# Performance work log

Hardware: AMD Instinct MI355X
Metric: run time of the kernel (lower is better)

## Reference

```python
import jax, jax.numpy as jnp
import numpy as np

NUM_NODES = 100000
NUM_EDGES = 1600000
NUM_GRAPHS = 1000
NUM_REP = 16
R_DIM = 16
N_SCALARS = 16
N_CLASSES = 6
N_LAYERS = 3
L_MAX = 1
EPS = 1e-8


def get_rot(v):
    """2x2 SO(2) rotation from 2D vector angle, L_max=1. v:[n,2] -> [n,1,2,2]."""
    theta = jnp.arctan2(v[:, 1], v[:, 0])
    c, s = jnp.cos(theta), jnp.sin(theta)
    R = jnp.stack([jnp.stack([c, -s], -1), jnp.stack([s, c], -1)], -2)  # [n,2,2]
    return R[:, None]  # [n, L_max=1, 2, 2]


def bessel(d, number=R_DIM, end=1.0):
    """Bessel radial basis sqrt(2/end)*sin(n*pi*d/end)/d. d:[E] -> [E,number]."""
    n = jnp.arange(1, number + 1, dtype=d.dtype)
    d_safe = d[:, None] + EPS
    return jnp.sqrt(2.0 / end) * jnp.sin(n * jnp.pi * d[:, None] / end) / d_safe


def seg_sum(x, idx, n):
    return jax.ops.segment_sum(x, idx, num_segments=n)


def setup_inputs() -> dict:
    key = jax.random.key(0)
    ks = jax.random.split(key, 20)
    pos = jax.random.normal(ks[0], (NUM_NODES, 2), dtype=jnp.float32)
    edge_index = jax.random.randint(ks[1], (2, NUM_EDGES), 0, NUM_NODES)
    batch = jnp.sort(jax.random.randint(ks[2], (NUM_NODES,), 0, NUM_GRAPHS))
    s = 0.1
    return {
        "pos": pos,
        "W_emb_rot": s * jax.random.normal(ks[3], (NUM_REP, L_MAX, 2), jnp.float32),
        "w_s_emb": s * jax.random.normal(ks[4], (N_SCALARS,), jnp.float32),
        "b_s_emb": jnp.zeros((N_SCALARS,), jnp.float32),
        "Wg": s * jax.random.normal(ks[5], (N_LAYERS, R_DIM, NUM_REP), jnp.float32),
        "bg": jnp.zeros((N_LAYERS, NUM_REP), jnp.float32),
        "Wmix": s * jax.random.normal(ks[6], (N_LAYERS, NUM_REP, NUM_REP), jnp.float32),
        "Wgate": s * jax.random.normal(ks[7], (N_LAYERS, N_SCALARS, NUM_REP), jnp.float32),
        "bgate": jnp.zeros((N_LAYERS, NUM_REP), jnp.float32),
        "Ws1": s * jax.random.normal(ks[8], (N_LAYERS, N_SCALARS + R_DIM, N_SCALARS), jnp.float32),
        "bs1": jnp.zeros((N_LAYERS, N_SCALARS), jnp.float32),
        "W1": s * jax.random.normal(ks[9], (N_SCALARS + NUM_REP * L_MAX * 2, 3 * (N_SCALARS + NUM_REP * L_MAX * 2)), jnp.float32),
        "b1": jnp.zeros((3 * (N_SCALARS + NUM_REP * L_MAX * 2),), jnp.float32),
        "W2": s * jax.random.normal(ks[10], (3 * (N_SCALARS + NUM_REP * L_MAX * 2), N_CLASSES), jnp.float32),
        "b2": jnp.zeros((N_CLASSES,), jnp.float32),
        "edge_index": edge_index,
        "batch": batch,
    }


def reference(pos, W_emb_rot, w_s_emb, b_s_emb, Wg, bg, Wmix, Wgate, bgate,
              Ws1, bs1, W1, b1, W2, b2, edge_index, batch):
    N = pos.shape[0]
    # --- geometry under no_grad in torch ---
    posg = jax.lax.stop_gradient(pos)
    cnt = seg_sum(jnp.ones((N,), posg.dtype), batch, NUM_GRAPHS)
    mean = seg_sum(posg, batch, NUM_GRAPHS) / jnp.maximum(cnt, 1.0)[:, None]
    posg = posg - mean[batch]
    rot_theta = get_rot(posg)                        # [N,1,2,2]
    row, col = edge_index[0], edge_index[1]
    edge_vec = posg[row] - posg[col]                 # [E,2]
    rot = get_rot(edge_vec)                          # [E,1,2,2]
    dist = jnp.linalg.norm(edge_vec, axis=1)         # [E]

    dist_emb = bessel(dist)                          # [E,r_dim]

    # --- edge embedding -> node features ---
    e_rot = jnp.einsum('eklm,jkm->ejkl', rot, W_emb_rot)      # [E,rep,1,2]
    deg = jnp.maximum(seg_sum(jnp.ones((row.shape[0],), pos.dtype), row, N), 1.0)
    x_rot = seg_sum(e_rot, row, N) / deg[:, None, None, None]  # [N,rep,1,2]
    d_mean = seg_sum(dist, row, N) / deg
    x_s = jax.nn.leaky_relu(d_mean[:, None] * w_s_emb[None, :] + b_s_emb)  # [N,ns]

    rot_inv = jnp.swapaxes(rot, -1, -2)
    # --- EqBlocks: gather -> rotate-in -> radial mix -> rotate-out -> scatter ---
    for i in range(N_LAYERS):
        local = jnp.einsum('eklm,ejkm->ejkl', rot_inv, x_rot[col])   # [E,rep,1,2]
        g = dist_emb @ Wg[i] + bg[i]                                 # [E,rep]
        local = jnp.einsum('ij,ejkl->eikl', Wmix[i], local) * g[:, :, None, None]
        msg = jnp.einsum('eklm,ejkm->ejkl', rot, local)              # [E,rep,1,2]
        agg = seg_sum(msg, row, N) / deg[:, None, None, None]
        gate = jax.nn.sigmoid(x_s @ Wgate[i] + bgate[i])             # [N,rep]
        x_rot = x_rot + agg * gate[:, :, None, None]
        msg_s = jax.nn.leaky_relu(
            jnp.concatenate([x_s[col], dist_emb], axis=1) @ Ws1[i] + bs1[i])
        x_s = x_s + seg_sum(msg_s, row, N) / deg[:, None]

    # --- SO2OutU (faithful to given source) ---
    rot_theta_inv = jnp.swapaxes(rot_theta, -1, -2)                  # [N,1,2,2]
    x_out = jnp.einsum('njkm,nkml->njkl', x_rot, rot_theta_inv)      # [N,rep,1,2]
    x_cat = jnp.concatenate([x_s, x_out.reshape(N, -1)], axis=1)    # [N,48]
    u = jax.nn.leaky_relu(x_cat @ W1 + b1) @ W2 + b2                 # [N,n_classes]
    return seg_sum(u, batch, NUM_GRAPHS)                             # [G,n_classes]
```

## Files before the change

kernel.cpp:

```cpp
#include <hip/hip_runtime.h>
#include <hip/hip_fp16.h>
#include <math.h>

#define NREP 16
#define RDIM 16
#define NS   16
#define NC   6
#define H1   144
#define DBINS 64
#define TILE 4096
#define P2CAP 10240

static __device__ __forceinline__ float leaky(float v) { return v > 0.0f ? v : 0.01f * v; }

__global__ void k_gsum_count(const float* __restrict__ pos, const int* __restrict__ batch,
                             int N, float* __restrict__ gsum, float* __restrict__ gcnt,
                             const int* __restrict__ ei, int E, int* __restrict__ cnt) {
  int t = threadIdx.x;
  int e = blockIdx.x * 256 + t;
  if (e < E) atomicAdd(&cnt[ei[e]], 1);

  __shared__ float bx[320], by[320], bc[320];
  int start = blockIdx.x * 256;
  if (start >= N) return;
  int n = start + t;
  int b0 = batch[min(start, N - 1)];
  int span = batch[min(start + 255, N - 1)] - b0;
  bool useLds = (span < 320);
  if (useLds) {
    for (int i = t; i <= span; i += 256) { bx[i] = 0.f; by[i] = 0.f; bc[i] = 0.f; }
    __syncthreads();
    if (n < N) {
      int rb = batch[n] - b0;
      atomicAdd(&bx[rb], pos[2 * n + 0]);
      atomicAdd(&by[rb], pos[2 * n + 1]);
      atomicAdd(&bc[rb], 1.0f);
    }
    __syncthreads();
    for (int i = t; i <= span; i += 256) {
      if (bc[i] != 0.0f) {
        atomicAdd(&gsum[2 * (b0 + i) + 0], bx[i]);
        atomicAdd(&gsum[2 * (b0 + i) + 1], by[i]);
        atomicAdd(&gcnt[b0 + i], bc[i]);
      }
    }
  } else if (n < N) {
    int b = batch[n];
    atomicAdd(&gsum[2 * b + 0], pos[2 * n + 0]);
    atomicAdd(&gsum[2 * b + 1], pos[2 * n + 1]);
    atomicAdd(&gcnt[b], 1.0f);
  }
}

__global__ void k_center_dhist_scan1(
    const float* __restrict__ pos, const int* __restrict__ batch, int N,
    const float* __restrict__ gsum, const float* __restrict__ gcnt,
    float* __restrict__ posc, float* __restrict__ cthn, float* __restrict__ sthn,
    const int* __restrict__ cnt, int* __restrict__ dhist,
    int* __restrict__ off, int* __restrict__ bsum) {
  __shared__ int lh[DBINS];
  __shared__ int sd[1024];
  int t = threadIdx.x;
  int i = blockIdx.x * 1024 + t;
  if (t < DBINS) lh[t] = 0;
  int v = (i < N) ? cnt[i] : 0;
  sd[t] = v;
  if (i < N) {
    int b = batch[i];
    float invc = 1.0f / fmaxf(gcnt[b], 1.0f);
    float px = pos[2 * i + 0] - gsum[2 * b + 0] * invc;
    float py = pos[2 * i + 1] - gsum[2 * b + 1] * invc;
    posc[2 * i + 0] = px;
    posc[2 * i + 1] = py;
    float r = sqrtf(px * px + py * py);
    if (r > 0.0f) { cthn[i] = px / r; sthn[i] = py / r; }
    else          { cthn[i] = 1.0f;  sthn[i] = 0.0f; }
  }
  __syncthreads();
  if (i < N) atomicAdd(&lh[min(v, DBINS - 1)], 1);
  for (int o = 1; o < 1024; o <<= 1) {
    int u = (t >= o) ? sd[t - o] : 0;
    __syncthreads();
    sd[t] += u;
    __syncthreads();
  }
  if (i < N) off[i] = sd[t] - v;
  if (t == 1023) bsum[blockIdx.x] = sd[1023];
  if (t < DBINS && lh[t] > 0) atomicAdd(&dhist[t], lh[t]);
}

__global__ void k_dscan_scan2(const int* __restrict__ dhist, int* __restrict__ dcur,
                              int* __restrict__ bsum, int nb) {
  __shared__ int s1[DBINS];
  __shared__ int s2[1024];
  int t = threadIdx.x;
  int v1 = (t < DBINS) ? dhist[t] : 0;
  if (t < DBINS) s1[t] = v1;
  int v2 = (t < nb) ? bsum[t] : 0;
  s2[t] = v2;
  __syncthreads();
  for (int o = 1; o < 1024; o <<= 1) {
    int u1 = (o < DBINS && t >= o && t < DBINS) ? s1[t - o] : 0;
    int u2 = (t >= o) ? s2[t - o] : 0;
    __syncthreads();
    if (o < DBINS && t < DBINS) s1[t] += u1;
    s2[t] += u2;
    __syncthreads();
  }
  if (t < DBINS) dcur[t] = s1[t] - v1;
  if (t < nb) bsum[t] = s2[t] - v2;
}

__global__ void k_dfill_scan3(int* __restrict__ off, const int* __restrict__ bsum,
                              int N, int E,
                              const int* __restrict__ cnt, int* __restrict__ dcur,
                              int* __restrict__ perm, int* __restrict__ cursor,
                              int* __restrict__ bcur) {
  int t = threadIdx.x;
  int i = blockIdx.x * 1024 + t;
  if (i < N) {
    int ov = off[i] + bsum[blockIdx.x];
    off[i] = ov;
    cursor[i] = ov;
    if ((i & 255) == 0) bcur[i >> 8] = ov;
  }
  if (i == N) off[N] = E;

  __shared__ int lh[DBINS];
  __shared__ int base[DBINS];
  if (t < DBINS) lh[t] = 0;
  __syncthreads();
  int b = 0, lr = 0;
  if (i < N) {
    b = min(cnt[i], DBINS - 1);
    lr = atomicAdd(&lh[b], 1);
  }
  __syncthreads();
  if (t < DBINS && lh[t] > 0) base[t] = atomicAdd(&dcur[t], lh[t]);
  __syncthreads();
  if (i < N) perm[base[b] + lr] = i;
}

__global__ void __launch_bounds__(256) k_part1(
    const int* __restrict__ ei, int E,
    int* __restrict__ bcur, long long* __restrict__ ebuf) {
  __shared__ int hist[512], lofs[512], gbase[512], pc[512];
  __shared__ long long stg[TILE];
  __shared__ unsigned short bkt[TILE];
  int t = threadIdx.x;
  int base = blockIdx.x * TILE;
  int cntt = min(TILE, E - base);
  for (int i = t; i < 512; i += 256) { hist[i] = 0; pc[i] = 0; }
  __syncthreads();
  int r[16], c[16];
#pragma unroll
  for (int i = 0; i < 16; i++) {
    int e = base + t + i * 256;
    r[i] = -1;
    if (e < E) {
      r[i] = ei[e];
      c[i] = ei[E + e];
      atomicAdd(&hist[r[i] >> 8], 1);
    }
  }
  __syncthreads();
  lofs[t] = hist[t]; lofs[t + 256] = hist[t + 256];
  __syncthreads();
  for (int o = 1; o < 512; o <<= 1) {
    int a0 = (t >= o) ? lofs[t - o] : 0;
    int a1 = lofs[t + 256 - o];
    __syncthreads();
    lofs[t] += a0; lofs[t + 256] += a1;
    __syncthreads();
  }
  int e0 = lofs[t] - hist[t], e1 = lofs[t + 256] - hist[t + 256];
  __syncthreads();
  lofs[t] = e0; lofs[t + 256] = e1;
  __syncthreads();
  for (int i = t; i < 512; i += 256)
    if (hist[i] > 0) gbase[i] = atomicAdd(&bcur[i], hist[i]);
  __syncthreads();
#pragma unroll
  for (int i = 0; i < 16; i++) {
    if (r[i] >= 0) {
      int b = r[i] >> 8;
      int l = lofs[b] + atomicAdd(&pc[b], 1);
      stg[l] = ((long long)r[i] << 32) | (unsigned int)c[i];
      bkt[l] = (unsigned short)b;
    }
  }
  __syncthreads();
  for (int j = t; j < cntt; j += 256) {
    int b = bkt[j];
    ebuf[gbase[b] + (j - lofs[b])] = stg[j];
  }
}

__global__ void __launch_bounds__(256) k_part2(
    const int* __restrict__ off, int N, const long long* __restrict__ ebuf,
    int* __restrict__ cursor, int* __restrict__ adj) {
  __shared__ int lcur[256];
  __shared__ int ladj[P2CAP];
  int t = threadIdx.x;
  int r0 = blockIdx.x << 8;
  int rend = min(r0 + 256, N);
  int abeg = off[r0];
  int aend = off[rend];
  int sz = aend - abeg;
  lcur[t] = (r0 + t < N) ? (off[r0 + t] - abeg) : 0;
  __syncthreads();
  if (sz <= P2CAP) {
    for (int j = abeg + t; j < aend; j += 256) {
      long long p = ebuf[j];
      int cl = (int)(unsigned int)(p & 0xffffffffLL);
      int rr = (int)(p >> 32);
      int l = atomicAdd(&lcur[rr - r0], 1);
      ladj[l] = cl;
    }
    __syncthreads();
    for (int j = t; j < sz; j += 256) adj[abeg + j] = ladj[j];
  } else {
    for (int j = abeg + t; j < aend; j += 256) {
      long long p = ebuf[j];
      int cl = (int)(unsigned int)(p & 0xffffffffLL);
      int rr = (int)(p >> 32);
      int l = atomicAdd(&cursor[rr], 1);
      adj[l] = cl;
    }
  }
}

__global__ void __launch_bounds__(256) k_init16(
    int N, const int* __restrict__ off, const int* __restrict__ adj,
    const float* __restrict__ posc, float2* __restrict__ spc,
    const float* __restrict__ Wer, const float* __restrict__ wse, const float* __restrict__ bse,
    const float* __restrict__ Wmix, const float* __restrict__ Ws1, const float* __restrict__ bs1,
    const float* __restrict__ Wgate, const float* __restrict__ bgate,
    float* __restrict__ xr, float* __restrict__ xs, uint2* __restrict__ yzg) {
  int idx = blockIdx.x * 256 + threadIdx.x;
  int n = idx >> 4, r = idx & 15;
  if (n >= N) return;
  int a = off[n], b = off[n + 1];
  float px = posc[2 * n + 0], py = posc[2 * n + 1];
  float C = 0.f, S = 0.f, D = 0.f;
  for (int k = a + r; k < b; k += 16) {
    int cl = adj[k];
    float dx = px - posc[2 * cl + 0];
    float dy = py - posc[2 * cl + 1];
    float d = sqrtf(dx * dx + dy * dy);
    float sp, cp;
    sincospif(d, &sp, &cp);
    float spp = 1.41421356237309515f * sp / (d + 1e-8f);
    spc[k] = make_float2(spp, 2.0f * cp);
    if (d > 0.0f) {
      float inv = 1.0f / d;
      C += dx * inv;
      S += dy * inv;
    } else {
      C += 1.0f;
    }
    D += d;
  }
#pragma unroll
  for (int o = 1; o < 16; o <<= 1) {
    C += __shfl_xor(C, o, 16);
    S += __shfl_xor(S, o, 16);
    D += __shfl_xor(D, o, 16);
  }
  float id = 1.0f / fmaxf((float)(b - a), 1.0f);
  C *= id; S *= id;
  float dm = D * id;
  float w0 = Wer[2 * r], w1 = Wer[2 * r + 1];
  float2 x;
  x.x = C * w0 - S * w1;
  x.y = S * w0 + C * w1;
  ((float2*)xr)[(size_t)n * 16 + r] = x;
  float s_new = leaky(dm * wse[r] + bse[r]);
  xs[(size_t)n * 16 + r] = s_new;

  float wmxn[16], wsan[16], wgtn[16];
#pragma unroll
  for (int q = 0; q < 16; q++) wmxn[q] = Wmix[r * 16 + q];
#pragma unroll
  for (int q = 0; q < 16; q++) wsan[q] = Ws1[q * 16 + r];
#pragma unroll
  for (int q = 0; q < 16; q++) wgtn[q] = Wgate[q * 16 + r];
  float y0 = 0.f, y1 = 0.f;
  float z = bs1[r], gtn = bgate[r];
#pragma unroll
  for (int j = 0; j < 16; j++) {
    float xj0 = __shfl(x.x, j, 16);
    float xj1 = __shfl(x.y, j, 16);
    float sj  = __shfl(s_new, j, 16);
    y0 += wmxn[j] * xj0;
    y1 += wmxn[j] * xj1;
    z  += wsan[j] * sj;
    gtn += wgtn[j] * sj;
  }
  gtn = 1.0f / (1.0f + __expf(-gtn));
  __half2 hA = __floats2half2_rn(y0, y1);
  __half2 hB = __floats2half2_rn(z, gtn);
  uint2 w2;
  w2.x = *(unsigned int*)&hA;
  w2.y = *(unsigned int*)&hB;
  yzg[(size_t)n * 16 + r] = w2;
}

__global__ void __launch_bounds__(256) k_layer(
    int N, const int* __restrict__ off,
    const int* __restrict__ adj, const float2* __restrict__ spc,
    const uint2* __restrict__ yzg, const int* __restrict__ perm,
    const float* __restrict__ Wg, const float* __restrict__ bg,
    const float* __restrict__ Ws1,
    float* xr, float* xs,
    int write_next, uint2* __restrict__ yzg_out,
    const float* __restrict__ Wmixn, const float* __restrict__ Ws1n,
    const float* __restrict__ bs1n,
    const float* __restrict__ Wgaten, const float* __restrict__ bgaten) {
  int idx = blockIdx.x * 256 + threadIdx.x;
  int g = idx >> 4, r = idx & 15;
  if (g >= N) return;
  int n = perm[g];
  float wg[16], ws[16];
#pragma unroll
  for (int q = 0; q < 16; q++) wg[q] = Wg[q * 16 + r];
#pragma unroll
  for (int q = 0; q < 16; q++) ws[q] = Ws1[(16 + q) * 16 + r];
  float bgr = bg[r];

  int a = off[n], bnd = off[n + 1];
  float acc0 = 0.f, acc1 = 0.f, accs = 0.f;
  if (a < bnd) {
    int last = bnd - 1;
    int    c0 = adj[a];               float2 p0 = spc[a];
    int    c1 = adj[min(a + 1, last)]; float2 p1 = spc[min(a + 1, last)];
    int    cn = adj[min(a + 2, last)]; float2 p2 = spc[min(a + 2, last)];
    uint2 Y0 = yzg[(c0 << 4) + r];
    uint2 Y1 = yzg[(c1 << 4) + r];
    int k = a;
    for (; k + 3 < bnd; k++) {
      int c3 = adj[k + 3];
      float2 p3 = spc[k + 3];
      uint2 Y2 = yzg[(cn << 4) + r];
      float skm1 = 0.f, sk = p0.x, c2 = p0.y;
      float g1 = bgr, dot = 0.f;
#pragma unroll
      for (int q = 0; q < RDIM; q++) {
        g1  = __builtin_fmaf(sk, wg[q], g1);
        dot = __builtin_fmaf(sk, ws[q], dot);
        float sn = __builtin_fmaf(c2, sk, -skm1);
        skm1 = sk; sk = sn;
      }
      float2 f01 = __half22float2(*(__half2*)&Y0.x);
      float2 fzg = __half22float2(*(__half2*)&Y0.y);
      acc0 = __builtin_fmaf(g1, f01.x, acc0);
      acc1 = __builtin_fmaf(g1, f01.y, acc1);
      accs += leaky(dot + fzg.x);
      c0 = c1; p0 = p1; c1 = cn; p1 = p2; cn = c3; p2 = p3; Y0 = Y1; Y1 = Y2;
    }
    for (; k < bnd; k++) {
      uint2 Y2 = Y1;
      if (k + 2 < bnd) Y2 = yzg[(cn << 4) + r];
      float skm1 = 0.f, sk = p0.x, c2 = p0.y;
      float g1 = bgr, dot = 0.f;
#pragma unroll
      for (int q = 0; q < RDIM; q++) {
        g1  = __builtin_fmaf(sk, wg[q], g1);
        dot = __builtin_fmaf(sk, ws[q], dot);
        float sn = __builtin_fmaf(c2, sk, -skm1);
        skm1 = sk; sk = sn;
      }
      float2 f01 = __half22float2(*(__half2*)&Y0.x);
      float2 fzg = __half22float2(*(__half2*)&Y0.y);
      acc0 = __builtin_fmaf(g1, f01.x, acc0);
      acc1 = __builtin_fmaf(g1, f01.y, acc1);
      accs += leaky(dot + fzg.x);
      c0 = c1; p0 = p1; c1 = cn; p1 = p2; Y0 = Y1; Y1 = Y2;
    }
  }
  float id = 1.0f / fmaxf((float)(bnd - a), 1.0f);
  uint2 Yg = yzg[(n << 4) + r];
  float gt = __half22float2(*(__half2*)&Yg.y).y;
  float2* xr2 = (float2*)xr;
  float2 x = xr2[(n << 4) + r];
  x.x += acc0 * id * gt;
  x.y += acc1 * id * gt;
  xr2[(n << 4) + r] = x;
  float s_new = xs[(n << 4) + r] + accs * id;
  xs[(n << 4) + r] = s_new;

  if (write_next) {
    float wmxn[16], wsan[16], wgtn[16];
#pragma unroll
    for (int q = 0; q < 16; q++) wmxn[q] = Wmixn[r * 16 + q];
#pragma unroll
    for (int q = 0; q < 16; q++) wsan[q] = Ws1n[q * 16 + r];
#pragma unroll
    for (int q = 0; q < 16; q++) wgtn[q] = Wgaten[q * 16 + r];
    float y0 = 0.f, y1 = 0.f;
    float z = bs1n[r], gtn = bgaten[r];
#pragma unroll
    for (int j = 0; j < 16; j++) {
      float xj0 = __shfl(x.x, j, 16);
      float xj1 = __shfl(x.y, j, 16);
      float sj  = __shfl(s_new, j, 16);
      y0 += wmxn[j] * xj0;
      y1 += wmxn[j] * xj1;
      z  += wsan[j] * sj;
      gtn += wgtn[j] * sj;
    }
    gtn = 1.0f / (1.0f + __expf(-gtn));
    __half2 hA = __floats2half2_rn(y0, y1);
    __half2 hB = __floats2half2_rn(z, gtn);
    uint2 w2;
    w2.x = *(unsigned int*)&hA;
    w2.y = *(unsigned int*)&hB;
    yzg_out[(n << 4) + r] = w2;
  }
}

__global__ void __launch_bounds__(128) k_final(
    int N, const float* __restrict__ xr, const float* __restrict__ xs,
    const float* __restrict__ cthn, const float* __restrict__ sthn,
    const int* __restrict__ batch,
    const float* __restrict__ W1, const float* __restrict__ b1,
    const float* __restrict__ W2, const float* __restrict__ b2,
    float* __restrict__ out) {
  __shared__ float obin[320 * 6];
  int t = threadIdx.x;
  int start = blockIdx.x * 128;
  int n = start + t;
  int b0 = batch[min(start, N - 1)];
  int span = batch[min(start + 127, N - 1)] - b0;
  bool useLds = (span < 320);
  if (useLds) for (int i = t; i < (span + 1) * 6; i += 128) obin[i] = 0.f;
  __syncthreads();

  float u[NC];
  bool act = (n < N);
  if (act) {
    float xc[48];
    const float4* xs4 = (const float4*)(xs + (size_t)n * NS);
#pragma unroll
    for (int j = 0; j < 4; j++) {
      float4 v = xs4[j];
      xc[4 * j + 0] = v.x; xc[4 * j + 1] = v.y; xc[4 * j + 2] = v.z; xc[4 * j + 3] = v.w;
    }
    float c = cthn[n], s = sthn[n];
    const float4* xr4 = (const float4*)(xr + (size_t)n * 32);
#pragma unroll
    for (int j = 0; j < 8; j++) {
      float4 v = xr4[j];
      xc[16 + 4 * j + 0] = c * v.x - s * v.y;
      xc[16 + 4 * j + 1] = s * v.x + c * v.y;
      xc[16 + 4 * j + 2] = c * v.z - s * v.w;
      xc[16 + 4 * j + 3] = s * v.z + c * v.w;
    }
#pragma unroll
    for (int q = 0; q < NC; q++) u[q] = b2[q];
    for (int h = 0; h < H1; h += 4) {
      float a0 = b1[h + 0], a1 = b1[h + 1], a2 = b1[h + 2], a3 = b1[h + 3];
#pragma unroll
      for (int q = 0; q < 48; q++) {
        float4 w = *(const float4*)(W1 + (size_t)q * H1 + h);
        float x = xc[q];
        a0 = __builtin_fmaf(x, w.x, a0);
        a1 = __builtin_fmaf(x, w.y, a1);
        a2 = __builtin_fmaf(x, w.z, a2);
        a3 = __builtin_fmaf(x, w.w, a3);
      }
      a0 = leaky(a0); a1 = leaky(a1); a2 = leaky(a2); a3 = leaky(a3);
#pragma unroll
      for (int q = 0; q < NC; q++)
        u[q] += a0 * W2[(h + 0) * 6 + q] + a1 * W2[(h + 1) * 6 + q]
              + a2 * W2[(h + 2) * 6 + q] + a3 * W2[(h + 3) * 6 + q];
    }
  }
  if (useLds) {
    if (act) {
      int rb = batch[n] - b0;
#pragma unroll
      for (int q = 0; q < NC; q++) atomicAdd(&obin[rb * 6 + q], u[q]);
    }
    __syncthreads();
    for (int i = t; i < (span + 1) * 6; i += 128) atomicAdd(&out[b0 * 6 + i], obin[i]);
  } else if (act) {
    int b = batch[n];
#pragma unroll
    for (int q = 0; q < NC; q++) atomicAdd(&out[b * 6 + q], u[q]);
  }
}

extern "C" void kernel_launch(void* const* d_in, const int* in_sizes, int n_in,
                              void* d_out, int out_size, void* d_ws, size_t ws_size,
                              hipStream_t stream) {
  const float* pos   = (const float*)d_in[0];
  const float* Wer   = (const float*)d_in[1];
  const float* wse   = (const float*)d_in[2];
  const float* bse   = (const float*)d_in[3];
  const float* Wg    = (const float*)d_in[4];
  const float* bg    = (const float*)d_in[5];
  const float* Wmix  = (const float*)d_in[6];
  const float* Wgate = (const float*)d_in[7];
  const float* bgate = (const float*)d_in[8];
  const float* Ws1   = (const float*)d_in[9];
  const float* bs1   = (const float*)d_in[10];
  const float* W1    = (const float*)d_in[11];
  const float* b1    = (const float*)d_in[12];
  const float* W2    = (const float*)d_in[13];
  const float* b2    = (const float*)d_in[14];
  const int*   ei    = (const int*)d_in[15];
  const int*   batch = (const int*)d_in[16];
  float* out = (float*)d_out;

  int N = in_sizes[0] / 2;
  int E = in_sizes[15] / 2;
  int G = out_size / NC;

  float* W = (float*)d_ws;
  size_t o = 0;
  float* gsum   = W + o; o += (size_t)2 * G;
  float* gcnt   = W + o; o += (size_t)G;
  int*   cnt    = (int*)(W + o); o += (size_t)N;
  int*   cursor = (int*)(W + o); o += (size_t)N;
  int*   dhist  = (int*)(W + o); o += (size_t)DBINS;
  size_t zero_bytes = o * 4;
  o = (o + 3) & ~(size_t)3;
  float* posc   = W + o; o += (size_t)2 * N;
  float* cthn   = W + o; o += (size_t)N;
  float* sthn   = W + o; o += (size_t)N;
  int*   off    = (int*)(W + o); o += (size_t)N + 1; o = (o + 3) & ~(size_t)3;
  int*   bsum   = (int*)(W + o); o += (size_t)1024;
  int*   dcur   = (int*)(W + o); o += (size_t)DBINS;
  int*   bcur   = (int*)(W + o); o += (size_t)512;
  int*   perm   = (int*)(W + o); o += (size_t)N; o = (o + 3) & ~(size_t)3;
  int*   adj    = (int*)(W + o); o += (size_t)E; o = (o + 1) & ~(size_t)1;
  float2* spc   = (float2*)(W + o); o += (size_t)2 * E;
  long long* ebuf = (long long*)spc;
  uint2* yzgA   = (uint2*)(W + o); o += (size_t)32 * N;
  uint2* yzgB   = (uint2*)(W + o); o += (size_t)32 * N;
  float* xr     = W + o; o += (size_t)N * 32;
  float* xs     = W + o; o += (size_t)N * 16;
  (void)ws_size;

  hipMemsetAsync(d_ws, 0, zero_bytes, stream);
  hipMemsetAsync(d_out, 0, (size_t)out_size * 4, stream);

  int nbE  = (E + 255) / 256;
  int nbN16 = ((size_t)N * 16 + 255) / 256;
  int nbS  = (N + 1023) / 1024;
  int nbS3 = (N + 1 + 1023) / 1024;
  int nbF  = (N + 127) / 128;
  int nbP1 = (E + TILE - 1) / TILE;
  int nbP2 = (N + 255) / 256;

  k_gsum_count<<<nbE, 256, 0, stream>>>(pos, batch, N, gsum, gcnt, ei, E, cnt);
  k_center_dhist_scan1<<<nbS, 1024, 0, stream>>>(pos, batch, N, gsum, gcnt,
                                                 posc, cthn, sthn, cnt, dhist, off, bsum);
  k_dscan_scan2<<<1, 1024, 0, stream>>>(dhist, dcur, bsum, nbS);
  k_dfill_scan3<<<nbS3, 1024, 0, stream>>>(off, bsum, N, E, cnt, dcur, perm, cursor, bcur);
  k_part1<<<nbP1, 256, 0, stream>>>(ei, E, bcur, ebuf);
  k_part2<<<nbP2, 256, 0, stream>>>(off, N, ebuf, cursor, adj);
  k_init16<<<nbN16, 256, 0, stream>>>(N, off, adj, posc, spc, Wer, wse, bse,
                                      Wmix, Ws1, bs1, Wgate, bgate,
                                      xr, xs, yzgA);

  k_layer<<<nbN16, 256, 0, stream>>>(N, off, adj, spc, yzgA, perm,
                                     Wg, bg, Ws1, xr, xs,
                                     1, yzgB,
                                     Wmix + 256, Ws1 + 512, bs1 + 16, Wgate + 256, bgate + 16);
  k_layer<<<nbN16, 256, 0, stream>>>(N, off, adj, spc, yzgB, perm,
                                     Wg + 256, bg + 16, Ws1 + 512, xr, xs,
                                     1, yzgA,
                                     Wmix + 512, Ws1 + 1024, bs1 + 32, Wgate + 512, bgate + 32);
  k_layer<<<nbN16, 256, 0, stream>>>(N, off, adj, spc, yzgA, perm,
                                     Wg + 512, bg + 32, Ws1 + 1024, xr, xs,
                                     0, yzgB,
                                     Wmix, Ws1, bs1, Wgate, bgate);

  k_final<<<nbF, 128, 0, stream>>>(N, xr, xs, cthn, sthn, batch, W1, b1, W2, b2, out);
}
```

Before: 491.0 us.

## Restructure CSR build around 256-row buckets and fuse node init into partition

```diff
diff --git a/kernel.cpp b/kernel.cpp
--- a/kernel.cpp
+++ b/kernel.cpp
@@ -9,16 +9,25 @@
 #define H1   144
 #define DBINS 64
 #define TILE 4096
+#define NBMAX 512
 #define P2CAP 10240
 
 static __device__ __forceinline__ float leaky(float v) { return v > 0.0f ? v : 0.01f * v; }
 
-__global__ void k_gsum_count(const float* __restrict__ pos, const int* __restrict__ batch,
-                             int N, float* __restrict__ gsum, float* __restrict__ gcnt,
-                             const int* __restrict__ ei, int E, int* __restrict__ cnt) {
+__global__ void __launch_bounds__(256) k_gsum_bhist(
+    const float* __restrict__ pos, const int* __restrict__ batch, int N,
+    float* __restrict__ gsum, float* __restrict__ gcnt,
+    const int* __restrict__ ei, int E, int* __restrict__ bhist) {
   int t = threadIdx.x;
-  int e = blockIdx.x * 256 + t;
-  if (e < E) atomicAdd(&cnt[ei[e]], 1);
+  __shared__ int h[NBMAX];
+  for (int i = t; i < NBMAX; i += 256) h[i] = 0;
+  __syncthreads();
+  int base = blockIdx.x * TILE;
+  int lim = min(base + TILE, E);
+  for (int j = base + t; j < lim; j += 256) atomicAdd(&h[ei[j] >> 8], 1);
+  __syncthreads();
+  for (int i = t; i < NBMAX; i += 256)
+    if (h[i] > 0) atomicAdd(&bhist[i], h[i]);
 
   __shared__ float bx[320], by[320], bc[320];
   int start = blockIdx.x * 256;
@@ -52,19 +61,30 @@
   }
 }
 
-__global__ void k_center_dhist_scan1(
-    const float* __restrict__ pos, const int* __restrict__ batch, int N,
+__global__ void __launch_bounds__(256) k_center_bscan(
+    const float* __restrict__ pos, const int* __restrict__ batch, int N, int E,
     const float* __restrict__ gsum, const float* __restrict__ gcnt,
     float* __restrict__ posc, float* __restrict__ cthn, float* __restrict__ sthn,
-    const int* __restrict__ cnt, int* __restrict__ dhist,
-    int* __restrict__ off, int* __restrict__ bsum) {
-  __shared__ int lh[DBINS];
-  __shared__ int sd[1024];
+    const int* __restrict__ bhist, int* __restrict__ bbase, int* __restrict__ bcur, int NB) {
   int t = threadIdx.x;
-  int i = blockIdx.x * 1024 + t;
-  if (t < DBINS) lh[t] = 0;
-  int v = (i < N) ? cnt[i] : 0;
-  sd[t] = v;
+  if (blockIdx.x == 0) {
+    __shared__ int s[NBMAX];
+    int v0 = (t < NB) ? bhist[t] : 0;
+    int v1 = (t + 256 < NB) ? bhist[t + 256] : 0;
+    s[t] = v0; s[t + 256] = v1;
+    __syncthreads();
+    for (int o = 1; o < NBMAX; o <<= 1) {
+      int a0 = (t >= o) ? s[t - o] : 0;
+      int a1 = s[t + 256 - o];
+      __syncthreads();
+      s[t] += a0; s[t + 256] += a1;
+      __syncthreads();
+    }
+    if (t < NB)       { int ex = s[t] - v0;       bbase[t] = ex;       bcur[t] = ex; }
+    if (t + 256 < NB) { int ex = s[t + 256] - v1; bbase[t + 256] = ex; bcur[t + 256] = ex; }
+    if (t == 0) bbase[NB] = E;
+  }
+  int i = blockIdx.x * 256 + t;
   if (i < N) {
     int b = batch[i];
     float invc = 1.0f / fmaxf(gcnt[b], 1.0f);
@@ -76,81 +96,18 @@
     if (r > 0.0f) { cthn[i] = px / r; sthn[i] = py / r; }
     else          { cthn[i] = 1.0f;  sthn[i] = 0.0f; }
   }
-  __syncthreads();
-  if (i < N) atomicAdd(&lh[min(v, DBINS - 1)], 1);
-  for (int o = 1; o < 1024; o <<= 1) {
-    int u = (t >= o) ? sd[t - o] : 0;
-    __syncthreads();
-    sd[t] += u;
-    __syncthreads();
-  }
-  if (i < N) off[i] = sd[t] - v;
-  if (t == 1023) bsum[blockIdx.x] = sd[1023];
-  if (t < DBINS && lh[t] > 0) atomicAdd(&dhist[t], lh[t]);
-}
-
-__global__ void k_dscan_scan2(const int* __restrict__ dhist, int* __restrict__ dcur,
-                              int* __restrict__ bsum, int nb) {
-  __shared__ int s1[DBINS];
-  __shared__ int s2[1024];
-  int t = threadIdx.x;
-  int v1 = (t < DBINS) ? dhist[t] : 0;
-  if (t < DBINS) s1[t] = v1;
-  int v2 = (t < nb) ? bsum[t] : 0;
-  s2[t] = v2;
-  __syncthreads();
-  for (int o = 1; o < 1024; o <<= 1) {
-    int u1 = (o < DBINS && t >= o && t < DBINS) ? s1[t - o] : 0;
-    int u2 = (t >= o) ? s2[t - o] : 0;
-    __syncthreads();
-    if (o < DBINS && t < DBINS) s1[t] += u1;
-    s2[t] += u2;
-    __syncthreads();
-  }
-  if (t < DBINS) dcur[t] = s1[t] - v1;
-  if (t < nb) bsum[t] = s2[t] - v2;
-}
-
-__global__ void k_dfill_scan3(int* __restrict__ off, const int* __restrict__ bsum,
-                              int N, int E,
-                              const int* __restrict__ cnt, int* __restrict__ dcur,
-                              int* __restrict__ perm, int* __restrict__ cursor,
-                              int* __restrict__ bcur) {
-  int t = threadIdx.x;
-  int i = blockIdx.x * 1024 + t;
-  if (i < N) {
-    int ov = off[i] + bsum[blockIdx.x];
-    off[i] = ov;
-    cursor[i] = ov;
-    if ((i & 255) == 0) bcur[i >> 8] = ov;
-  }
-  if (i == N) off[N] = E;
-
-  __shared__ int lh[DBINS];
-  __shared__ int base[DBINS];
-  if (t < DBINS) lh[t] = 0;
-  __syncthreads();
-  int b = 0, lr = 0;
-  if (i < N) {
-    b = min(cnt[i], DBINS - 1);
-    lr = atomicAdd(&lh[b], 1);
-  }
-  __syncthreads();
-  if (t < DBINS && lh[t] > 0) base[t] = atomicAdd(&dcur[t], lh[t]);
-  __syncthreads();
-  if (i < N) perm[base[b] + lr] = i;
 }
 
 __global__ void __launch_bounds__(256) k_part1(
     const int* __restrict__ ei, int E,
     int* __restrict__ bcur, long long* __restrict__ ebuf) {
-  __shared__ int hist[512], lofs[512], gbase[512], pc[512];
+  __shared__ int hist[NBMAX], lofs[NBMAX], gbase[NBMAX], pc[NBMAX];
   __shared__ long long stg[TILE];
   __shared__ unsigned short bkt[TILE];
   int t = threadIdx.x;
   int base = blockIdx.x * TILE;
   int cntt = min(TILE, E - base);
-  for (int i = t; i < 512; i += 256) { hist[i] = 0; pc[i] = 0; }
+  for (int i = t; i < NBMAX; i += 256) { hist[i] = 0; pc[i] = 0; }
   __syncthreads();
   int r[16], c[16];
 #pragma unroll
@@ -166,7 +123,7 @@
   __syncthreads();
   lofs[t] = hist[t]; lofs[t + 256] = hist[t + 256];
   __syncthreads();
-  for (int o = 1; o < 512; o <<= 1) {
+  for (int o = 1; o < NBMAX; o <<= 1) {
     int a0 = (t >= o) ? lofs[t - o] : 0;
     int a1 = lofs[t + 256 - o];
     __syncthreads();
@@ -177,7 +134,7 @@
   __syncthreads();
   lofs[t] = e0; lofs[t + 256] = e1;
   __syncthreads();
-  for (int i = t; i < 512; i += 256)
+  for (int i = t; i < NBMAX; i += 256)
     if (hist[i] > 0) gbase[i] = atomicAdd(&bcur[i], hist[i]);
   __syncthreads();
 #pragma unroll
@@ -196,114 +153,172 @@
   }
 }
 
-__global__ void __launch_bounds__(256) k_part2(
-    const int* __restrict__ off, int N, const long long* __restrict__ ebuf,
-    int* __restrict__ cursor, int* __restrict__ adj) {
-  __shared__ int lcur[256];
+__global__ void __launch_bounds__(256) k_part2i(
+    const int* __restrict__ bbase, int N, int E,
+    const long long* __restrict__ ebuf,
+    const float* __restrict__ posc,
+    int* __restrict__ off, int* __restrict__ cnt, int* __restrict__ dhist,
+    int* __restrict__ adj, float2* __restrict__ spc,
+    const float* __restrict__ Wer, const float* __restrict__ wse, const float* __restrict__ bse,
+    const float* __restrict__ Wmix, const float* __restrict__ Ws1, const float* __restrict__ bs1,
+    const float* __restrict__ Wgate, const float* __restrict__ bgate,
+    float* __restrict__ xr, float* __restrict__ xs, uint2* __restrict__ yzg) {
+  __shared__ int lcnt[256], loff[256], lcur[256];
+  __shared__ float lC[256], lS[256], lD[256], lpx[256], lpy[256];
+  __shared__ int lh[DBINS];
   __shared__ int ladj[P2CAP];
+  __shared__ unsigned char lrow[P2CAP];
   int t = threadIdx.x;
-  int r0 = blockIdx.x << 8;
-  int rend = min(r0 + 256, N);
-  int abeg = off[r0];
-  int aend = off[rend];
+  int b = blockIdx.x;
+  int r0 = b << 8;
+  int abeg = bbase[b];
+  int aend = bbase[b + 1];
   int sz = aend - abeg;
-  lcur[t] = (r0 + t < N) ? (off[r0 + t] - abeg) : 0;
-  __syncthreads();
+  bool haveRow = (r0 + t < N);
+  lcnt[t] = 0;
+  lC[t] = 0.f; lS[t] = 0.f; lD[t] = 0.f;
+  if (t < DBINS) lh[t] = 0;
+  if (haveRow) { lpx[t] = posc[2 * (r0 + t)]; lpy[t] = posc[2 * (r0 + t) + 1]; }
+  __syncthreads();
+  for (int j = abeg + t; j < aend; j += 256)
+    atomicAdd(&lcnt[(int)(ebuf[j] >> 32) - r0], 1);
+  __syncthreads();
+  int v = lcnt[t];
+  loff[t] = v;
+  __syncthreads();
+  for (int o = 1; o < 256; o <<= 1) {
+    int u = (t >= o) ? loff[t - o] : 0;
+    __syncthreads();
+    loff[t] += u;
+    __syncthreads();
+  }
+  int myoff = loff[t] - v;
+  __syncthreads();
+  loff[t] = myoff;
+  lcur[t] = myoff;
+  if (haveRow) {
+    off[r0 + t] = abeg + myoff;
+    cnt[r0 + t] = v;
+    atomicAdd(&lh[min(v, DBINS - 1)], 1);
+  }
+  if (t == 0 && r0 + 256 >= N) off[N] = E;
+  __syncthreads();
+  if (t < DBINS && lh[t] > 0) atomicAdd(&dhist[t], lh[t]);
   if (sz <= P2CAP) {
     for (int j = abeg + t; j < aend; j += 256) {
       long long p = ebuf[j];
       int cl = (int)(unsigned int)(p & 0xffffffffLL);
-      int rr = (int)(p >> 32);
-      int l = atomicAdd(&lcur[rr - r0], 1);
+      int rr = (int)(p >> 32) - r0;
+      int l = atomicAdd(&lcur[rr], 1);
       ladj[l] = cl;
-    }
-    __syncthreads();
-    for (int j = t; j < sz; j += 256) adj[abeg + j] = ladj[j];
+      lrow[l] = (unsigned char)rr;
+    }
+    __syncthreads();
+    for (int k = t; k < sz; k += 256) {
+      int cl = ladj[k];
+      int rr = lrow[k];
+      adj[abeg + k] = cl;
+      float dx = lpx[rr] - posc[2 * cl + 0];
+      float dy = lpy[rr] - posc[2 * cl + 1];
+      float d = sqrtf(dx * dx + dy * dy);
+      float sp, cp;
+      sincospif(d, &sp, &cp);
+      spc[abeg + k] = make_float2(1.41421356237309515f * sp / (d + 1e-8f), 2.0f * cp);
+      float invd = (d > 0.f) ? 1.f / d : 0.f;
+      atomicAdd(&lC[rr], (d > 0.f) ? dx * invd : 1.0f);
+      atomicAdd(&lS[rr], dy * invd);
+      atomicAdd(&lD[rr], d);
+    }
   } else {
     for (int j = abeg + t; j < aend; j += 256) {
       long long p = ebuf[j];
       int cl = (int)(unsigned int)(p & 0xffffffffLL);
-      int rr = (int)(p >> 32);
-      int l = atomicAdd(&cursor[rr], 1);
+      int rr = (int)(p >> 32) - r0;
+      int l = abeg + atomicAdd(&lcur[rr], 1);
       adj[l] = cl;
-    }
-  }
-}
-
-__global__ void __launch_bounds__(256) k_init16(
-    int N, const int* __restrict__ off, const int* __restrict__ adj,
-    const float* __restrict__ posc, float2* __restrict__ spc,
-    const float* __restrict__ Wer, const float* __restrict__ wse, const float* __restrict__ bse,
-    const float* __restrict__ Wmix, const float* __restrict__ Ws1, const float* __restrict__ bs1,
-    const float* __restrict__ Wgate, const float* __restrict__ bgate,
-    float* __restrict__ xr, float* __restrict__ xs, uint2* __restrict__ yzg) {
-  int idx = blockIdx.x * 256 + threadIdx.x;
-  int n = idx >> 4, r = idx & 15;
-  if (n >= N) return;
-  int a = off[n], b = off[n + 1];
-  float px = posc[2 * n + 0], py = posc[2 * n + 1];
-  float C = 0.f, S = 0.f, D = 0.f;
-  for (int k = a + r; k < b; k += 16) {
-    int cl = adj[k];
-    float dx = px - posc[2 * cl + 0];
-    float dy = py - posc[2 * cl + 1];
-    float d = sqrtf(dx * dx + dy * dy);
-    float sp, cp;
-    sincospif(d, &sp, &cp);
-    float spp = 1.41421356237309515f * sp / (d + 1e-8f);
-    spc[k] = make_float2(spp, 2.0f * cp);
-    if (d > 0.0f) {
-      float inv = 1.0f / d;
-      C += dx * inv;
-      S += dy * inv;
-    } else {
-      C += 1.0f;
-    }
-    D += d;
-  }
-#pragma unroll
-  for (int o = 1; o < 16; o <<= 1) {
-    C += __shfl_xor(C, o, 16);
-    S += __shfl_xor(S, o, 16);
-    D += __shfl_xor(D, o, 16);
-  }
-  float id = 1.0f / fmaxf((float)(b - a), 1.0f);
-  C *= id; S *= id;
-  float dm = D * id;
+      float dx = lpx[rr] - posc[2 * cl + 0];
+      float dy = lpy[rr] - posc[2 * cl + 1];
+      float d = sqrtf(dx * dx + dy * dy);
+      float sp, cp;
+      sincospif(d, &sp, &cp);
+      spc[l] = make_float2(1.41421356237309515f * sp / (d + 1e-8f), 2.0f * cp);
+      float invd = (d > 0.f) ? 1.f / d : 0.f;
+      atomicAdd(&lC[rr], (d > 0.f) ? dx * invd : 1.0f);
+      atomicAdd(&lS[rr], dy * invd);
+      atomicAdd(&lD[rr], d);
+    }
+  }
+  __syncthreads();
+  int r = t & 15;
+  float wmxn[16], wsan[16], wgtn[16];
+#pragma unroll
+  for (int q = 0; q < 16; q++) wmxn[q] = Wmix[r * 16 + q];
+#pragma unroll
+  for (int q = 0; q < 16; q++) wsan[q] = Ws1[q * 16 + r];
+#pragma unroll
+  for (int q = 0; q < 16; q++) wgtn[q] = Wgate[q * 16 + r];
   float w0 = Wer[2 * r], w1 = Wer[2 * r + 1];
-  float2 x;
-  x.x = C * w0 - S * w1;
-  x.y = S * w0 + C * w1;
-  ((float2*)xr)[(size_t)n * 16 + r] = x;
-  float s_new = leaky(dm * wse[r] + bse[r]);
-  xs[(size_t)n * 16 + r] = s_new;
-
-  float wmxn[16], wsan[16], wgtn[16];
-#pragma unroll
-  for (int q = 0; q < 16; q++) wmxn[q] = Wmix[r * 16 + q];
-#pragma unroll
-  for (int q = 0; q < 16; q++) wsan[q] = Ws1[q * 16 + r];
-#pragma unroll
-  for (int q = 0; q < 16; q++) wgtn[q] = Wgate[q * 16 + r];
-  float y0 = 0.f, y1 = 0.f;
-  float z = bs1[r], gtn = bgate[r];
-#pragma unroll
-  for (int j = 0; j < 16; j++) {
-    float xj0 = __shfl(x.x, j, 16);
-    float xj1 = __shfl(x.y, j, 16);
-    float sj  = __shfl(s_new, j, 16);
-    y0 += wmxn[j] * xj0;
-    y1 += wmxn[j] * xj1;
-    z  += wsan[j] * sj;
-    gtn += wgtn[j] * sj;
-  }
-  gtn = 1.0f / (1.0f + __expf(-gtn));
-  __half2 hA = __floats2half2_rn(y0, y1);
-  __half2 hB = __floats2half2_rn(z, gtn);
-  uint2 w2;
-  w2.x = *(unsigned int*)&hA;
-  w2.y = *(unsigned int*)&hB;
-  yzg[(size_t)n * 16 + r] = w2;
+  for (int round = 0; round < 16; round++) {
+    int node = (round << 4) + (t >> 4);
+    int n = r0 + node;
+    if (n >= N) continue;
+    float id = 1.0f / fmaxf((float)lcnt[node], 1.0f);
+    float C = lC[node] * id, S = lS[node] * id, dm = lD[node] * id;
+    float2 x;
+    x.x = C * w0 - S * w1;
+    x.y = S * w0 + C * w1;
+    ((float2*)xr)[(size_t)n * 16 + r] = x;
+    float s_new = leaky(dm * wse[r] + bse[r]);
+    xs[(size_t)n * 16 + r] = s_new;
+    float y0 = 0.f, y1 = 0.f;
+    float z = bs1[r], gtn = bgate[r];
+#pragma unroll
+    for (int j = 0; j < 16; j++) {
+      float xj0 = __shfl(x.x, j, 16);
+      float xj1 = __shfl(x.y, j, 16);
+      float sj  = __shfl(s_new, j, 16);
+      y0 += wmxn[j] * xj0;
+      y1 += wmxn[j] * xj1;
+      z  += wsan[j] * sj;
+      gtn += wgtn[j] * sj;
+    }
+    gtn = 1.0f / (1.0f + __expf(-gtn));
+    __half2 hA = __floats2half2_rn(y0, y1);
+    __half2 hB = __floats2half2_rn(z, gtn);
+    uint2 w2;
+    w2.x = *(unsigned int*)&hA;
+    w2.y = *(unsigned int*)&hB;
+    yzg[(size_t)n * 16 + r] = w2;
+  }
+}
+
+__global__ void k_permfill(int N, const int* __restrict__ cnt,
+                           const int* __restrict__ dhist,
+                           int* __restrict__ dcur, int* __restrict__ perm) {
+  __shared__ int sd[DBINS], dbase[DBINS];
+  __shared__ int lh[DBINS], base[DBINS];
+  int t = threadIdx.x;
+  int dv = 0;
+  if (t < DBINS) { dv = dhist[t]; sd[t] = dv; lh[t] = 0; }
+  __syncthreads();
+  for (int o = 1; o < DBINS; o <<= 1) {
+    int u = (t >= o && t < DBINS) ? sd[t - o] : 0;
+    __syncthreads();
+    if (t < DBINS) sd[t] += u;
+    __syncthreads();
+  }
+  if (t < DBINS) dbase[t] = sd[t] - dv;
+  __syncthreads();
+  int i = blockIdx.x * 1024 + t;
+  int b = 0, lr = 0;
+  if (i < N) {
+    b = min(cnt[i], DBINS - 1);
+    lr = atomicAdd(&lh[b], 1);
+  }
+  __syncthreads();
+  if (t < DBINS && lh[t] > 0) base[t] = dbase[t] + atomicAdd(&dcur[t], lh[t]);
+  __syncthreads();
+  if (i < N) perm[base[b] + lr] = i;
 }
 
 __global__ void __launch_bounds__(256) k_layer(
@@ -516,23 +531,24 @@
   int N = in_sizes[0] / 2;
   int E = in_sizes[15] / 2;
   int G = out_size / NC;
+  int NB = (N + 255) / 256;
 
   float* W = (float*)d_ws;
   size_t o = 0;
   float* gsum   = W + o; o += (size_t)2 * G;
   float* gcnt   = W + o; o += (size_t)G;
-  int*   cnt    = (int*)(W + o); o += (size_t)N;
-  int*   cursor = (int*)(W + o); o += (size_t)N;
+  int*   bhist  = (int*)(W + o); o += (size_t)NBMAX;
   int*   dhist  = (int*)(W + o); o += (size_t)DBINS;
+  int*   dcur   = (int*)(W + o); o += (size_t)DBINS;
   size_t zero_bytes = o * 4;
   o = (o + 3) & ~(size_t)3;
   float* posc   = W + o; o += (size_t)2 * N;
   float* cthn   = W + o; o += (size_t)N;
   float* sthn   = W + o; o += (size_t)N;
   int*   off    = (int*)(W + o); o += (size_t)N + 1; o = (o + 3) & ~(size_t)3;
-  int*   bsum   = (int*)(W + o); o += (size_t)1024;
-  int*   dcur   = (int*)(W + o); o += (size_t)DBINS;
-  int*   bcur   = (int*)(W + o); o += (size_t)512;
+  int*   bbase  = (int*)(W + o); o += (size_t)NBMAX + 1;
+  int*   bcur   = (int*)(W + o); o += (size_t)NBMAX;
+  int*   cnt    = (int*)(W + o); o += (size_t)N;
   int*   perm   = (int*)(W + o); o += (size_t)N; o = (o + 3) & ~(size_t)3;
   int*   adj    = (int*)(W + o); o += (size_t)E; o = (o + 1) & ~(size_t)1;
   float2* spc   = (float2*)(W + o); o += (size_t)2 * E;
@@ -546,24 +562,22 @@
   hipMemsetAsync(d_ws, 0, zero_bytes, stream);
   hipMemsetAsync(d_out, 0, (size_t)out_size * 4, stream);
 
-  int nbE  = (E + 255) / 256;
+  int nbN  = (N + 255) / 256;
+  int nbT  = (E + TILE - 1) / TILE;
+  int nbG  = nbT > nbN ? nbT : nbN;
   int nbN16 = ((size_t)N * 16 + 255) / 256;
-  int nbS  = (N + 1023) / 1024;
-  int nbS3 = (N + 1 + 1023) / 1024;
+  int nbP  = (N + 1023) / 1024;
   int nbF  = (N + 127) / 128;
-  int nbP1 = (E + TILE - 1) / TILE;
-  int nbP2 = (N + 255) / 256;
-
-  k_gsum_count<<<nbE, 256, 0, stream>>>(pos, batch, N, gsum, gcnt, ei, E, cnt);
-  k_center_dhist_scan1<<<nbS, 1024, 0, stream>>>(pos, batch, N, gsum, gcnt,
-                                                 posc, cthn, sthn, cnt, dhist, off, bsum);
-  k_dscan_scan2<<<1, 1024, 0, stream>>>(dhist, dcur, bsum, nbS);
-  k_dfill_scan3<<<nbS3, 1024, 0, stream>>>(off, bsum, N, E, cnt, dcur, perm, cursor, bcur);
-  k_part1<<<nbP1, 256, 0, stream>>>(ei, E, bcur, ebuf);
-  k_part2<<<nbP2, 256, 0, stream>>>(off, N, ebuf, cursor, adj);
-  k_init16<<<nbN16, 256, 0, stream>>>(N, off, adj, posc, spc, Wer, wse, bse,
-                                      Wmix, Ws1, bs1, Wgate, bgate,
-                                      xr, xs, yzgA);
+
+  k_gsum_bhist<<<nbG, 256, 0, stream>>>(pos, batch, N, gsum, gcnt, ei, E, bhist);
+  k_center_bscan<<<nbN, 256, 0, stream>>>(pos, batch, N, E, gsum, gcnt,
+                                          posc, cthn, sthn, bhist, bbase, bcur, NB);
+  k_part1<<<nbT, 256, 0, stream>>>(ei, E, bcur, ebuf);
+  k_part2i<<<NB, 256, 0, stream>>>(bbase, N, E, ebuf, posc,
+                                   off, cnt, dhist, adj, spc,
+                                   Wer, wse, bse, Wmix, Ws1, bs1, Wgate, bgate,
+                                   xr, xs, yzgA);
+  k_permfill<<<nbP, 1024, 0, stream>>>(N, cnt, dhist, dcur, perm);
 
   k_layer<<<nbN16, 256, 0, stream>>>(N, off, adj, spc, yzgA, perm,
                                      Wg, bg, Ws1, xr, xs,
```

Measured after the change: 446.2 us. 1.1x faster.
